# Performance work log

Hardware: AMD Instinct MI355X
Metric: run time of the kernel (lower is better)

Reference implementation:

```python
import jax, jax.numpy as jnp
import numpy as np
import math

# geometry: ROI [-140.8,-40,-3,140.8,40,1], grid 0.4 -> (Z,Y,X)=(10,200,704)
B_AG = 2              # total agents = 1 sample x 2 agents
Z, Y, X = 10, 200, 704
Z1, Y1, X1 = 5, 100, 352   # after stride-2 conv (k=3, p=1)
N_PTS = 10000         # active radar voxels per agent
C_IN, C0, C1 = 64, 32, 64
N_IN = B_AG * N_PTS
CAP0 = 27 * N_IN                # padded bound on spconv0 active outputs
CAP1 = B_AG * Z1 * Y1 * X1      # padded bound on spconv1 active outputs
EPS = 1e-5

_OFFS = np.array([[a, b, c] for a in range(3) for b in range(3) for c in range(3)])


def _spconv_rulebook(coords, stride, zyx, pair_cap, out_cap):
    """Rulebook for SparseConv3d k=3 pad=1. coords [N,4]=(b,z,y,x).
    Returns gather [27,P], scatter [27,P] (dummy=out_cap), out coords padded
    to out_cap (pad coords are out-of-bounds so dense scatter drops them)."""
    oz, oy, ox = zyx
    per_in, per_lin = [], []
    for off in _OFFS:
        t = coords[:, 1:] + 1 - off
        ok = (t % stride == 0).all(1)
        o = t // stride
        ok &= (o >= 0).all(1) & (o[:, 0] < oz) & (o[:, 1] < oy) & (o[:, 2] < ox)
        idx = np.nonzero(ok)[0]
        oc = o[idx]
        per_in.append(idx)
        per_lin.append(((coords[idx, 0] * oz + oc[:, 0]) * oy + oc[:, 1]) * ox + oc[:, 2])
    all_lin = np.unique(np.concatenate(per_lin))
    n_out = len(all_lin)
    g = np.zeros((27, pair_cap), np.int32)
    s = np.full((27, pair_cap), out_cap, np.int32)
    for k in range(27):
        n = len(per_in[k])
        g[k, :n] = per_in[k]
        s[k, :n] = np.searchsorted(all_lin, per_lin[k])
    b = all_lin // (oz * oy * ox); r = all_lin % (oz * oy * ox)
    zc = r // (oy * ox); r = r % (oy * ox)
    out_coords = np.stack([b, zc, r // ox, r % ox], 1).astype(np.int32)
    pad = np.zeros((out_cap - n_out, 4), np.int32); pad[:, 1] = oz  # OOB -> dropped
    return g, s, np.concatenate([out_coords, pad], 0), n_out


def _subm_rulebook(coords, n_act, zyx, pair_cap, out_cap):
    """SubMConv3d k=3: same active set in/out; coords[:n_act] sorted by lin id."""
    oz, oy, ox = zyx
    c = coords[:n_act]
    lins = ((c[:, 0] * oz + c[:, 1]) * oy + c[:, 2]) * ox + c[:, 3]
    g = np.zeros((27, pair_cap), np.int32)
    s = np.full((27, pair_cap), out_cap, np.int32)
    for k, off in enumerate(_OFFS):
        cand = c[:, 1:] + (off - 1)
        ok = (cand >= 0).all(1) & (cand[:, 0] < oz) & (cand[:, 1] < oy) & (cand[:, 2] < ox)
        cl = ((c[:, 0] * oz + cand[:, 0]) * oy + cand[:, 1]) * ox + cand[:, 2]
        pos = np.minimum(np.searchsorted(lins, cl), n_act - 1)
        ok &= lins[pos] == cl
        idx = np.nonzero(ok)[0]
        g[k, :len(idx)] = pos[idx]
        s[k, :len(idx)] = idx
    return g, s


def setup_inputs() -> dict:
    rng = np.random.default_rng(0)
    cl = []
    for b in range(B_AG):
        lin = np.sort(rng.choice(Z * Y * X, N_PTS, replace=False))
        z = lin // (Y * X); r = lin % (Y * X)
        cl.append(np.stack([np.full(N_PTS, b), z, r // X, r % X], 1))
    coords_in = np.concatenate(cl, 0).astype(np.int64)

    g0, s0, coords0, n0 = _spconv_rulebook(coords_in, 1, (Z, Y, X), N_IN, CAP0)
    ga, sa = _subm_rulebook(coords0, n0, (Z, Y, X), CAP0, CAP0)
    g1, s1, coords1, n1 = _spconv_rulebook(coords0[:n0], 2, (Z1, Y1, X1), CAP0, CAP1)
    gb, sb = _subm_rulebook(coords1, n1, (Z1, Y1, X1), CAP1, CAP1)

    ks = jax.random.split(jax.random.key(0), 20)
    f32 = jnp.float32
    def W(k, *shape, fan):
        return jax.random.normal(k, shape, f32) * (1.0 / np.sqrt(fan))
    def bn(k, c):  # [gamma, beta, running_mean, running_var]
        m = jax.random.normal(k, (c,), f32) * 0.1
        v = 1.0 + jax.random.uniform(jax.random.fold_in(k, 1), (c,), f32)
        return jnp.stack([jnp.ones((c,), f32), jnp.zeros((c,), f32), m, v])
    return dict(
        sp_feats=jax.random.normal(ks[0], (N_IN, C_IN), f32),
        w_in=W(ks[1], C_IN, C0, fan=C_IN),
        w0=W(ks[2], 27, C0, C0, fan=27 * C0), bnp0=bn(ks[3], C0),
        w0a=W(ks[4], 27, C0, C0, fan=27 * C0), bnp0a=bn(ks[5], C0),
        w0b=W(ks[6], 27, C0, C0, fan=27 * C0), bnp0b=bn(ks[7], C0),
        w1=W(ks[8], 27, C0, C1, fan=27 * C0), bnp1=bn(ks[9], C1),
        w1a=W(ks[10], 27, C1, C1, fan=27 * C1), bnp1a=bn(ks[11], C1),
        w1b=W(ks[12], 27, C1, C1, fan=27 * C1), bnp1b=bn(ks[13], C1),
        ct0_w=W(ks[14], C0 * Z, 64, 1, 1, fan=C0 * Z), ct0_b=jnp.zeros((64,), f32),
        bnt0=bn(ks[15], 64),
        ct1_w=W(ks[16], C1 * Z1, 64, 2, 2, fan=C1 * Z1 * 4), ct1_b=jnp.zeros((64,), f32),
        bnt1=bn(ks[17], 64),
        coords0=jnp.asarray(coords0), coords1=jnp.asarray(coords1),
        g0=jnp.asarray(g0), s0=jnp.asarray(s0),
        ga=jnp.asarray(ga), sa=jnp.asarray(sa),
        g1=jnp.asarray(g1), s1=jnp.asarray(s1),
        gb=jnp.asarray(gb), sb=jnp.asarray(sb),
        record_len=2,
    )


def _bn1d(x, p):  # x [N,C]; p [4,C]
    g, b, m, v = p
    return (x - m) * (g * jax.lax.rsqrt(v + EPS)) + b


def _bn2d(x, p):  # x [B,C,H,W]
    g, b, m, v = (t[:, None, None] for t in p)
    return (x - m) * (g * jax.lax.rsqrt(v + EPS)) + b


def _spconv(feats, g, s, W, out_cap):
    """gather-GEMM-scatter: feats [Nin,Cin], g/s [27,P], W [27,Cin,Cout]."""
    out = jnp.zeros((out_cap + 1, W.shape[2]), feats.dtype)  # +1 dummy row
    for k in range(27):
        out = out.at[s[k]].add(feats[g[k]] @ W[k])
    return out[:out_cap]


def _to_dense(feats, coords, b, z, y, x):
    d = jnp.zeros((b, z, y, x, feats.shape[1]), feats.dtype)
    d = d.at[coords[:, 0], coords[:, 1], coords[:, 2], coords[:, 3]].add(feats)
    return d.transpose(0, 4, 1, 2, 3)  # B,C,Z,Y,X


def _conv_t2d(x, w, b, stride, pad):
    """torch ConvTranspose2d; w [Cin,Cout,k,k]."""
    k = w.shape[2]
    wf = jnp.flip(w, (2, 3)).transpose(1, 0, 2, 3)  # Cout,Cin,k,k
    out = jax.lax.conv_general_dilated(
        x, wf, window_strides=(1, 1),
        padding=[(k - 1 - pad, k - 1 - pad)] * 2,
        lhs_dilation=(stride, stride),
        dimension_numbers=('NCHW', 'OIHW', 'NCHW'))
    return out + b[None, :, None, None]


def _att_fusion(x, L):
    """OpenCOOD AttFusion: per-pixel scaled dot-product attention over agents,
    keep ego (agent 0). Assumes uniform record_len == L."""
    B, C, H, Wd = x.shape
    S = B // L
    xr = x.reshape(S, L, C, H * Wd).transpose(0, 3, 1, 2)  # S,HW,L,C
    att = jax.nn.softmax(jnp.einsum('snlc,snmc->snlm', xr, xr) / math.sqrt(C), -1)
    h = jnp.einsum('snlm,snmc->snlc', att, xr)[:, :, 0, :]  # ego agent
    return h.transpose(0, 2, 1).reshape(S, C, H, Wd)


def reference(sp_feats, w_in, w0, bnp0, w0a, bnp0a, w0b, bnp0b,
              w1, bnp1, w1a, bnp1a, w1b, bnp1b,
              ct0_w, ct0_b, bnt0, ct1_w, ct1_b, bnt1,
              coords0, coords1, g0, s0, ga, sa, g1, s1, gb, sb, record_len):
    relu = jax.nn.relu
    f = sp_feats @ w_in                         # input_conv (k=1)
    # ---- encoder layer 0 (stride 1) ----
    f = relu(_bn1d(_spconv(f, g0, s0, w0, CAP0), bnp0))
    f = relu(_bn1d(_spconv(f, ga, sa, w0a, CAP0), bnp0a))
    f = relu(_bn1d(_spconv(f, ga, sa, w0b, CAP0), bnp0b))
    d0 = _to_dense(f, coords0, B_AG, Z, Y, X).reshape(B_AG, C0 * Z, Y, X)  # b (c z) y x
    bev0 = relu(_bn2d(_conv_t2d(d0, ct0_w, ct0_b, 1, 0), bnt0))
    bev0 = _att_fusion(bev0, record_len)
    # ---- encoder layer 1 (stride 2) ----
    f = relu(_bn1d(_spconv(f, g1, s1, w1, CAP1), bnp1))
    f = relu(_bn1d(_spconv(f, gb, sb, w1a, CAP1), bnp1a))
    f = relu(_bn1d(_spconv(f, gb, sb, w1b, CAP1), bnp1b))
    d1 = _to_dense(f, coords1, B_AG, Z1, Y1, X1).reshape(B_AG, C1 * Z1, Y1, X1)
    bev1 = relu(_bn2d(_conv_t2d(d1, ct1_w, ct1_b, 2, 0), bnt1))
    bev1 = _att_fusion(bev1, record_len)
    return jnp.concatenate([bev0, bev1], axis=1)  # [S, 128, 200, 704]
```

## Files before the change

### kernel.cpp

```cpp
#include <hip/hip_runtime.h>
#include <hip/hip_bf16.h>
#include <hip/hip_fp16.h>

#define N_PTS_IN   20000
#define CAP0C      540000
#define CAP1C      352000
#define ZD 10
#define YD 200
#define XD 704
#define Z1D 5
#define Y1D 100
#define X1D 352
#define HWOUT (YD*XD)

typedef _Float16 f16x8 __attribute__((ext_vector_type(8)));
typedef float    f32x4 __attribute__((ext_vector_type(4)));

__global__ __launch_bounds__(256) void gemm_in(const float* __restrict__ sp,
                                               const float* __restrict__ w,
                                               __half* __restrict__ fout) {
    int tid = blockIdx.x * 256 + threadIdx.x;
    int row = tid >> 3;
    int c4  = (tid & 7) * 4;
    if (row >= N_PTS_IN) return;
    float4 acc = {0.f, 0.f, 0.f, 0.f};
    const float* sr = sp + (size_t)row * 64;
#pragma unroll
    for (int ci = 0; ci < 64; ci += 4) {
        float4 fv = *(const float4*)(sr + ci);
        const float* wp = w + ci * 32 + c4;
        float4 w0 = *(const float4*)(wp);
        float4 w1 = *(const float4*)(wp + 32);
        float4 w2 = *(const float4*)(wp + 64);
        float4 w3 = *(const float4*)(wp + 96);
        acc.x += fv.x*w0.x + fv.y*w1.x + fv.z*w2.x + fv.w*w3.x;
        acc.y += fv.x*w0.y + fv.y*w1.y + fv.z*w2.y + fv.w*w3.y;
        acc.z += fv.x*w0.z + fv.y*w1.z + fv.z*w2.z + fv.w*w3.z;
        acc.w += fv.x*w0.w + fv.y*w1.w + fv.z*w2.w + fv.w*w3.w;
    }
    __half* fo = fout + (size_t)row * 32 + c4;
    fo[0] = __float2half(acc.x);
    fo[1] = __float2half(acc.y);
    fo[2] = __float2half(acc.z);
    fo[3] = __float2half(acc.w);
}

__global__ __launch_bounds__(256) void cvt_w(const float* __restrict__ src,
                                             __half* __restrict__ dst,
                                             int CIN, int COUT) {
    int i = blockIdx.x * 256 + threadIdx.x;
    if (i >= 27 * CIN * COUT) return;
    int ci = i % CIN;
    int t  = i / CIN;
    int co = t % COUT;
    int k  = t / COUT;
    dst[i] = __float2half(src[((size_t)k * CIN + ci) * COUT + co]);
}

__global__ __launch_bounds__(256) void cvt_ct0(const float* __restrict__ src,
                                               __half* __restrict__ dst) {
    int i = blockIdx.x * 256 + threadIdx.x;
    if (i >= 64 * 320) return;
    int zc = i % 320, co = i / 320;
    int z = zc >> 5, c = zc & 31;
    dst[i] = __float2half(src[(c * 10 + z) * 64 + co]);
}

__global__ __launch_bounds__(256) void cvt_ct1(const float* __restrict__ src,
                                               __half* __restrict__ dst) {
    int i = blockIdx.x * 256 + threadIdx.x;
    if (i >= 4 * 64 * 320) return;
    int zc = i % 320;
    int t  = i / 320;
    int co = t & 63;
    int kq = t >> 6;
    int z = zc >> 6, c = zc & 63;
    dst[i] = __float2half(src[((c * 5 + z) * 64 + co) * 4 + kq]);
}

__global__ __launch_bounds__(256) void build_nbr(const int* __restrict__ g,
                                                 const int* __restrict__ s,
                                                 int* __restrict__ nbrT,
                                                 int P, int cap) {
    int i = blockIdx.x * 256 + threadIdx.x;
    if (i >= 27 * P) return;
    int k = i / P, p = i - k * P;
    int sv = s[(size_t)k * P + p];
    if (sv >= cap) return;
    nbrT[(size_t)k * cap + sv] = g[(size_t)k * P + p];
}

__global__ __launch_bounds__(128) void find_nact(const int* __restrict__ c0,
                                                 const int* __restrict__ c1,
                                                 int* __restrict__ nA) {
    int t = threadIdx.x;
    if (t == 0) {
        int lo = 0, hi = CAP0C;
        while (lo < hi) {
            int mid = (lo + hi) >> 1;
            if (c0[4 * mid + 1] >= ZD) hi = mid; else lo = mid + 1;
        }
        nA[0] = lo;
    } else if (t == 64) {
        int lo = 0, hi = CAP1C;
        while (lo < hi) {
            int mid = (lo + hi) >> 1;
            if (c1[4 * mid + 1] >= Z1D) hi = mid; else lo = mid + 1;
        }
        nA[1] = lo;
    }
}

__global__ __launch_bounds__(256) void build_vox(const int* __restrict__ coords,
                                                 int* __restrict__ v2r,
                                                 int cap, int Zdim, int Ydim, int Xdim) {
    int r = blockIdx.x * 256 + threadIdx.x;
    if (r >= cap) return;
    int b = coords[4*r], z = coords[4*r+1], y = coords[4*r+2], x = coords[4*r+3];
    if (z >= Zdim) return;
    v2r[(((size_t)b * Zdim + z) * Ydim + y) * Xdim + x] = r;
}

template <int CIN, int COUT>
__global__ __launch_bounds__(256) void spconv_reg(const __half* __restrict__ f,
                                                  const __half* __restrict__ wt,
                                                  const float* __restrict__ bnp,
                                                  const int* __restrict__ nbrT,
                                                  __half* __restrict__ fout,
                                                  int ncap,
                                                  const int* __restrict__ nA) {
    constexpr int NT = COUT / 16;
    constexpr int KT = CIN / 32;
    constexpr int NCHUNK = CIN / 8;
    constexpr int MASK = NCHUNK - 1;
    constexpr int LCH  = (NCHUNK == 8) ? 3 : 2;
    constexpr int TILE_H = COUT * CIN;
    constexpr int TB = TILE_H * 2 / 256;
    constexpr int OST_H = 4 * 32 * COUT;
    constexpr int SH_H = (2 * TILE_H > OST_H) ? 2 * TILE_H : OST_H;
    __shared__ __align__(16) __half S[SH_H];

    int tid = threadIdx.x;
    int wv = tid >> 6, lane = tid & 63;
    int quad = lane >> 4, l16 = lane & 15;

    int bid = blockIdx.x;
    int nfull = (int)gridDim.x & ~63;
    int sb;
    if (bid < nfull) {
        int grp = bid >> 6, w = bid & 63;
        sb = grp * 64 + (w & 7) * 8 + (w >> 3);
    } else {
        sb = bid;
    }

    if (sb * 128 >= *nA) return;

    int m0 = sb * 128 + wv * 32;
    int r0 = m0 + l16;
    int r1 = m0 + 16 + l16;
    bool ok0 = r0 < ncap, ok1 = r1 < ncap;

    f32x4 acc[2][NT] = {};

    int gC0 = ok0 ? nbrT[r0] : -1;
    int gC1 = ok1 ? nbrT[r1] : -1;
    int gN0 = ok0 ? nbrT[(size_t)ncap + r0] : -1;
    int gN1 = ok1 ? nbrT[(size_t)ncap + r1] : -1;
    bool anyC = __ballot((gC0 >= 0) || (gC1 >= 0)) != 0ull;
    bool ever = false;

    f16x8 aC0[KT], aC1[KT];
#pragma unroll
    for (int kt = 0; kt < KT; ++kt) {
        uint4 z4 = {0u,0u,0u,0u};
        aC0[kt] = *(f16x8*)&z4;
        aC1[kt] = *(f16x8*)&z4;
    }
    if (anyC) {
        const __half* p0 = f + (size_t)((gC0 < 0) ? 0 : gC0) * CIN + quad * 8;
        const __half* p1 = f + (size_t)((gC1 < 0) ? 0 : gC1) * CIN + quad * 8;
#pragma unroll
        for (int kt = 0; kt < KT; ++kt) {
            uint4 u0 = {0u,0u,0u,0u}, u1 = {0u,0u,0u,0u};
            if (gC0 >= 0) u0 = *(const uint4*)(p0 + kt * 32);
            if (gC1 >= 0) u1 = *(const uint4*)(p1 + kt * 32);
            aC0[kt] = *(f16x8*)&u0;
            aC1[kt] = *(f16x8*)&u1;
        }
    }

    {
        const char* src = (const char*)(wt) + tid * TB;
        if constexpr (TB == 32) {
            uint4 w0 = *(const uint4*)src;
            uint4 w1 = *(const uint4*)(src + 16);
            int p0 = tid * 2;
#pragma unroll
            for (int j = 0; j < 2; ++j) {
                int p = p0 + j;
                int row = p >> LCH, c = p & MASK;
                *(uint4*)(S + (row * NCHUNK + (c ^ (row & MASK))) * 8) = (j ? w1 : w0);
            }
        } else if constexpr (TB == 16) {
            uint4 w0 = *(const uint4*)src;
            int p = tid;
            int row = p >> LCH, c = p & MASK;
            *(uint4*)(S + (row * NCHUNK + (c ^ (row & MASK))) * 8) = w0;
        } else {
            uint2 w0 = *(const uint2*)src;
            int p = tid >> 1, half = tid & 1;
            int row = p >> LCH, c = p & MASK;
            *(uint2*)(S + (row * NCHUNK + (c ^ (row & MASK))) * 8 + half * 4) = w0;
        }
    }
    __syncthreads();

#pragma unroll 1
    for (int k = 0; k < 27; ++k) {
        int gNN0 = -1, gNN1 = -1;
        if (k + 2 < 27) {
            if (ok0) gNN0 = nbrT[(size_t)(k + 2) * ncap + r0];
            if (ok1) gNN1 = nbrT[(size_t)(k + 2) * ncap + r1];
        }
        bool anyN = __ballot((gN0 >= 0) || (gN1 >= 0)) != 0ull;
        f16x8 aN0[KT], aN1[KT];
#pragma unroll
        for (int kt = 0; kt < KT; ++kt) {
            uint4 z4 = {0u,0u,0u,0u};
            aN0[kt] = *(f16x8*)&z4;
            aN1[kt] = *(f16x8*)&z4;
        }
        if (anyN) {
            const __half* p0 = f + (size_t)((gN0 < 0) ? 0 : gN0) * CIN + quad * 8;
            const __half* p1 = f + (size_t)((gN1 < 0) ? 0 : gN1) * CIN + quad * 8;
#pragma unroll
            for (int kt = 0; kt < KT; ++kt) {
                uint4 u0 = {0u,0u,0u,0u}, u1 = {0u,0u,0u,0u};
                if (gN0 >= 0) u0 = *(const uint4*)(p0 + kt * 32);
                if (gN1 >= 0) u1 = *(const uint4*)(p1 + kt * 32);
                aN0[kt] = *(f16x8*)&u0;
                aN1[kt] = *(f16x8*)&u1;
            }
        }
        bool doStage = (k + 1 < 27);
        uint4 w0{}, w1{}; uint2 w2{};
        if (doStage) {
            const char* src = (const char*)(wt + (size_t)(k + 1) * TILE_H) + tid * TB;
            if constexpr (TB == 32)      { w0 = *(const uint4*)src; w1 = *(const uint4*)(src + 16); }
            else if constexpr (TB == 16) { w0 = *(const uint4*)src; }
            else                         { w2 = *(const uint2*)src; }
        }
        if (anyC) {
            ever = true;
            const __half* Wb = S + (k & 1) * TILE_H;
#pragma unroll
            for (int kt = 0; kt < KT; ++kt) {
#pragma unroll
                for (int nt = 0; nt < NT; ++nt) {
                    int row = nt * 16 + l16;
                    int c   = kt * 4 + quad;
                    f16x8 b = *(const f16x8*)(Wb + (row * NCHUNK + (c ^ (row & MASK))) * 8);
                    acc[0][nt] = __builtin_amdgcn_mfma_f32_16x16x32_f16(aC0[kt], b, acc[0][nt], 0, 0, 0);
                    acc[1][nt] = __builtin_amdgcn_mfma_f32_16x16x32_f16(aC1[kt], b, acc[1][nt], 0, 0, 0);
                }
            }
        }
        if (doStage) {
            __half* dst = S + ((k + 1) & 1) * TILE_H;
            if constexpr (TB == 32) {
                int p0 = tid * 2;
#pragma unroll
                for (int j = 0; j < 2; ++j) {
                    int p = p0 + j;
                    int row = p >> LCH, c = p & MASK;
                    *(uint4*)(dst + (row * NCHUNK + (c ^ (row & MASK))) * 8) = (j ? w1 : w0);
                }
            } else if constexpr (TB == 16) {
                int p = tid;
                int row = p >> LCH, c = p & MASK;
                *(uint4*)(dst + (row * NCHUNK + (c ^ (row & MASK))) * 8) = w0;
            } else {
                int p = tid >> 1, half = tid & 1;
                int row = p >> LCH, c = p & MASK;
                *(uint2*)(dst + (row * NCHUNK + (c ^ (row & MASK))) * 8 + half * 4) = w2;
            }
        }
        asm volatile("s_waitcnt lgkmcnt(0)" ::: "memory");
        __builtin_amdgcn_s_barrier();
#pragma unroll
        for (int kt = 0; kt < KT; ++kt) { aC0[kt] = aN0[kt]; aC1[kt] = aN1[kt]; }
        anyC = anyN;
        gC0 = gN0; gC1 = gN1; gN0 = gNN0; gN1 = gNN1;
    }

    if (!ever) return;
    __half* O = S + wv * (32 * COUT);
#pragma unroll
    for (int nt = 0; nt < NT; ++nt) {
        int co = nt * 16 + l16;
        float g = bnp[co], b = bnp[COUT + co];
        float mn = bnp[2*COUT + co], vv = bnp[3*COUT + co];
        float s  = g * rsqrtf(vv + 1e-5f);
        float sh = b - mn * s;
#pragma unroll
        for (int m = 0; m < 2; ++m)
#pragma unroll
            for (int r_ = 0; r_ < 4; ++r_) {
                int row = m * 16 + quad * 4 + r_;
                O[row * COUT + co] = __float2half(fmaxf(acc[m][nt][r_] * s + sh, 0.f));
            }
    }
    constexpr int OCH = COUT / 8;
#pragma unroll
    for (int j = 0; j < 32 * OCH / 64; ++j) {
        int idx = j * 64 + lane;
        int r = idx / OCH, c = idx % OCH;
        if (m0 + r < ncap)
            *(uint4*)(fout + (size_t)(m0 + r) * COUT + c * 8) =
                *(const uint4*)(O + r * COUT + c * 8);
    }
}

__global__ __launch_bounds__(256) void bev0_mfma(const __half* __restrict__ f0,
                                                 const __half* __restrict__ wtT,
                                                 const float* __restrict__ bias,
                                                 const float* __restrict__ bnp,
                                                 const int* __restrict__ v2r,
                                                 float* __restrict__ out) {
    __shared__ float Ot[64][66];
    int tid = threadIdx.x;
    int y = blockIdx.x / 11, x0 = (blockIdx.x % 11) * 64;
    int wv = tid >> 6, lane = tid & 63;
    int quad = lane >> 4, l16 = lane & 15;

    int rz[2][10];
#pragma unroll
    for (int m = 0; m < 2; ++m) {
        int row = wv * 32 + m * 16 + l16;
        int b = row & 1, p = row >> 1;
#pragma unroll
        for (int z = 0; z < 10; ++z)
            rz[m][z] = v2r[((b * ZD + z) * YD + y) * XD + x0 + p];
    }

    f32x4 acc[2][4] = {};
    f16x8 aC[2], bC[4];
#pragma unroll
    for (int m = 0; m < 2; ++m) {
        uint4 u = {0u,0u,0u,0u};
        int r = rz[m][0];
        if (r >= 0) u = *(const uint4*)(f0 + (size_t)r * 32 + quad * 8);
        aC[m] = *(f16x8*)&u;
    }
#pragma unroll
    for (int nt = 0; nt < 4; ++nt)
        bC[nt] = *(const f16x8*)(wtT + (size_t)(nt * 16 + l16) * 320 + quad * 8);

#pragma unroll
    for (int ks = 0; ks < 10; ++ks) {
        f16x8 aN[2], bN[4];
        if (ks + 1 < 10) {
#pragma unroll
            for (int m = 0; m < 2; ++m) {
                uint4 u = {0u,0u,0u,0u};
                int r = rz[m][ks + 1];
                if (r >= 0) u = *(const uint4*)(f0 + (size_t)r * 32 + quad * 8);
                aN[m] = *(f16x8*)&u;
            }
#pragma unroll
            for (int nt = 0; nt < 4; ++nt)
                bN[nt] = *(const f16x8*)(wtT + (size_t)(nt * 16 + l16) * 320 + (ks + 1) * 32 + quad * 8);
        } else {
            uint4 z4 = {0u,0u,0u,0u};
#pragma unroll
            for (int m = 0; m < 2; ++m) aN[m] = *(f16x8*)&z4;
#pragma unroll
            for (int nt = 0; nt < 4; ++nt) bN[nt] = *(f16x8*)&z4;
        }
#pragma unroll
        for (int nt = 0; nt < 4; ++nt) {
            acc[0][nt] = __builtin_amdgcn_mfma_f32_16x16x32_f16(aC[0], bC[nt], acc[0][nt], 0, 0, 0);
            acc[1][nt] = __builtin_amdgcn_mfma_f32_16x16x32_f16(aC[1], bC[nt], acc[1][nt], 0, 0, 0);
        }
        aC[0] = aN[0]; aC[1] = aN[1];
#pragma unroll
        for (int nt = 0; nt < 4; ++nt) bC[nt] = bN[nt];
    }

#pragma unroll
    for (int nt = 0; nt < 4; ++nt) {
        int co = nt * 16 + l16;
        float s  = bnp[co] * rsqrtf(bnp[192 + co] + 1e-5f);
        float sh = (bias[co] - bnp[128 + co]) * s + bnp[64 + co];
#pragma unroll
        for (int m = 0; m < 2; ++m)
#pragma unroll
            for (int r_ = 0; r_ < 4; ++r_)
                acc[m][nt][r_] = fmaxf(acc[m][nt][r_] * s + sh, 0.f);
    }

#pragma unroll
    for (int m = 0; m < 2; ++m)
#pragma unroll
        for (int jj = 0; jj < 2; ++jj) {
            float s00 = 0.f, s01 = 0.f;
#pragma unroll
            for (int nt = 0; nt < 4; ++nt) {
                float xv0 = acc[m][nt][2 * jj], xv1 = acc[m][nt][2 * jj + 1];
                s00 += xv0 * xv0;
                s01 += xv0 * xv1;
            }
#pragma unroll
            for (int o = 8; o > 0; o >>= 1) {
                s00 += __shfl_xor(s00, o);
                s01 += __shfl_xor(s01, o);
            }
            float a0 = s00 * 0.125f, a1 = s01 * 0.125f;
            float mx = fmaxf(a0, a1);
            float e0 = expf(a0 - mx), e1 = expf(a1 - mx);
            float inv = 1.f / (e0 + e1);
            int pl = wv * 16 + m * 8 + quad * 2 + jj;
#pragma unroll
            for (int nt = 0; nt < 4; ++nt)
                Ot[nt * 16 + l16][pl] =
                    (e0 * acc[m][nt][2 * jj] + e1 * acc[m][nt][2 * jj + 1]) * inv;
        }
    __syncthreads();

#pragma unroll
    for (int i = 0; i < 16; ++i) {
        int idx = i * 256 + tid;
        int co = idx >> 6, px = idx & 63;
        out[(size_t)co * HWOUT + (size_t)y * XD + x0 + px] = Ot[co][px];
    }
}

__global__ __launch_bounds__(256) void bev1_mfma(const __half* __restrict__ f1,
                                                 const __half* __restrict__ wtT,
                                                 const float* __restrict__ bias,
                                                 const float* __restrict__ bnp,
                                                 const int* __restrict__ v2r,
                                                 float* __restrict__ out) {
    constexpr int WST = 328;
    __shared__ __align__(16) __half Wl[64 * WST];
    __shared__ float Ot[64][66];
    int tid = threadIdx.x;
    int bid = blockIdx.x;
    int ky = bid & 1;
    int t  = bid >> 1;
    int iy = t / 11, j0 = (t % 11) * 32;
    int wv = tid >> 6, lane = tid & 63;
    int quad = lane >> 4, l16 = lane & 15;

    int row = wv * 16 + l16;
    int b = row & 1, p = row >> 1;
    int rz[5];
#pragma unroll
    for (int z = 0; z < 5; ++z)
        rz[z] = v2r[((b * Z1D + z) * Y1D + iy) * X1D + j0 + p];

    f16x8 a[10];
#pragma unroll
    for (int ks = 0; ks < 10; ++ks) {
        int z = ks >> 1, hf = ks & 1;
        uint4 u = {0u,0u,0u,0u};
        int r = rz[z];
        if (r >= 0) u = *(const uint4*)(f1 + (size_t)r * 64 + hf * 32 + quad * 8);
        a[ks] = *(f16x8*)&u;
    }

    f32x4 acc[2][4] = {};
#pragma unroll 1
    for (int kx = 0; kx < 2; ++kx) {
        const __half* wk = wtT + (size_t)(ky * 2 + kx) * 64 * 320;
        if (kx) __syncthreads();
#pragma unroll
        for (int c = 0; c < 10; ++c) {
            int idx = c * 256 + tid;
            int r_ = idx / 40, col = idx % 40;
            uint4 v = *(const uint4*)(wk + r_ * 320 + col * 8);
            *(uint4*)(Wl + r_ * WST + col * 8) = v;
        }
        __syncthreads();
#pragma unroll
        for (int ks = 0; ks < 10; ++ks)
#pragma unroll
            for (int nt = 0; nt < 4; ++nt) {
                f16x8 bf = *(const f16x8*)(Wl + (nt * 16 + l16) * WST + ks * 32 + quad * 8);
                acc[kx][nt] = __builtin_amdgcn_mfma_f32_16x16x32_f16(a[ks], bf, acc[kx][nt], 0, 0, 0);
            }
    }

#pragma unroll
    for (int kx = 0; kx < 2; ++kx) {
#pragma unroll
        for (int nt = 0; nt < 4; ++nt) {
            int co = nt * 16 + l16;
            float s  = bnp[co] * rsqrtf(bnp[192 + co] + 1e-5f);
            float sh = (bias[co] - bnp[128 + co]) * s + bnp[64 + co];
#pragma unroll
            for (int r_ = 0; r_ < 4; ++r_)
                acc[kx][nt][r_] = fmaxf(acc[kx][nt][r_] * s + sh, 0.f);
        }
#pragma unroll
        for (int jj = 0; jj < 2; ++jj) {
            float s00 = 0.f, s01 = 0.f;
#pragma unroll
            for (int nt = 0; nt < 4; ++nt) {
                float xv0 = acc[kx][nt][2 * jj], xv1 = acc[kx][nt][2 * jj + 1];
                s00 += xv0 * xv0;
                s01 += xv0 * xv1;
            }
#pragma unroll
            for (int o = 8; o > 0; o >>= 1) {
                s00 += __shfl_xor(s00, o);
                s01 += __shfl_xor(s01, o);
            }
            float a0 = s00 * 0.125f, a1 = s01 * 0.125f;
            float mx = fmaxf(a0, a1);
            float e0 = expf(a0 - mx), e1 = expf(a1 - mx);
            float inv = 1.f / (e0 + e1);
            int pl = wv * 8 + quad * 2 + jj;
#pragma unroll
            for (int nt = 0; nt < 4; ++nt)
                Ot[nt * 16 + l16][2 * pl + kx] =
                    (e0 * acc[kx][nt][2 * jj] + e1 * acc[kx][nt][2 * jj + 1]) * inv;
        }
    }
    __syncthreads();

    int yo = 2 * iy + ky;
#pragma unroll
    for (int i = 0; i < 16; ++i) {
        int idx = i * 256 + tid;
        int co = idx >> 6, xx = idx & 63;
        out[(size_t)co * HWOUT + (size_t)yo * XD + 2 * j0 + xx] = Ot[co][xx];
    }
}

extern "C" void kernel_launch(void* const* d_in, const int* in_sizes, int n_in,
                              void* d_out, int out_size, void* d_ws, size_t ws_size,
                              hipStream_t stream) {
    const float* sp    = (const float*)d_in[0];
    const float* w_in  = (const float*)d_in[1];
    const float* w0    = (const float*)d_in[2];
    const float* bnp0  = (const float*)d_in[3];
    const float* w0a   = (const float*)d_in[4];
    const float* bnp0a = (const float*)d_in[5];
    const float* w0b   = (const float*)d_in[6];
    const float* bnp0b = (const float*)d_in[7];
    const float* w1    = (const float*)d_in[8];
    const float* bnp1  = (const float*)d_in[9];
    const float* w1a   = (const float*)d_in[10];
    const float* bnp1a = (const float*)d_in[11];
    const float* w1b   = (const float*)d_in[12];
    const float* bnp1b = (const float*)d_in[13];
    const float* ct0w  = (const float*)d_in[14];
    const float* ct0b  = (const float*)d_in[15];
    const float* bnt0  = (const float*)d_in[16];
    const float* ct1w  = (const float*)d_in[17];
    const float* ct1b  = (const float*)d_in[18];
    const float* bnt1  = (const float*)d_in[19];
    const int* coords0 = (const int*)d_in[20];
    const int* coords1 = (const int*)d_in[21];
    const int* g0 = (const int*)d_in[22];
    const int* s0 = (const int*)d_in[23];
    const int* ga = (const int*)d_in[24];
    const int* sa = (const int*)d_in[25];
    const int* g1 = (const int*)d_in[26];
    const int* s1 = (const int*)d_in[27];
    const int* gb = (const int*)d_in[28];
    const int* sb = (const int*)d_in[29];
    float* out = (float*)d_out;

    __half* fInH = (__half*)d_ws;
    __half* R1h  = fInH + 640000;
    __half* R2h  = R1h + 22528000;
    __half* wt0  = R2h + 22528000;
    __half* wt0a = wt0  + 27648;
    __half* wt0b = wt0a + 27648;
    __half* wt1  = wt0b + 27648;
    __half* wt1a = wt1  + 55296;
    __half* wt1b = wt1a + 110592;
    __half* wtT0 = wt1b + 110592;
    __half* wtT1 = wtT0 + 20480;
    int*   nbrT = (int*)(wtT1 + 81920);
    int*   v2r0 = nbrT;
    int*   v2r1 = nbrT + 2816000;
    int*   nAct = nbrT + 14580000;

    find_nact<<<1, 128, 0, stream>>>(coords0, coords1, nAct);
    cvt_w<<<(27*32*32 + 255) / 256, 256, 0, stream>>>(w0,  wt0,  32, 32);
    cvt_w<<<(27*32*32 + 255) / 256, 256, 0, stream>>>(w0a, wt0a, 32, 32);
    cvt_w<<<(27*32*32 + 255) / 256, 256, 0, stream>>>(w0b, wt0b, 32, 32);
    cvt_w<<<(27*32*64 + 255) / 256, 256, 0, stream>>>(w1,  wt1,  32, 64);
    cvt_w<<<(27*64*64 + 255) / 256, 256, 0, stream>>>(w1a, wt1a, 64, 64);
    cvt_w<<<(27*64*64 + 255) / 256, 256, 0, stream>>>(w1b, wt1b, 64, 64);
    cvt_ct0<<<(64*320 + 255) / 256, 256, 0, stream>>>(ct0w, wtT0);
    cvt_ct1<<<(4*64*320 + 255) / 256, 256, 0, stream>>>(ct1w, wtT1);

    gemm_in<<<(N_PTS_IN * 8 + 255) / 256, 256, 0, stream>>>(sp, w_in, fInH);

    hipMemsetAsync(nbrT, 0xFF, (size_t)CAP0C * 27 * 4, stream);
    build_nbr<<<(27 * N_PTS_IN + 255) / 256, 256, 0, stream>>>(g0, s0, nbrT, N_PTS_IN, CAP0C);
    spconv_reg<32, 32><<<(CAP0C + 127) / 128, 256, 0, stream>>>(fInH, wt0, bnp0, nbrT, R1h, CAP0C, nAct + 0);

    hipMemsetAsync(nbrT, 0xFF, (size_t)CAP0C * 27 * 4, stream);
    build_nbr<<<(27 * CAP0C + 255) / 256, 256, 0, stream>>>(ga, sa, nbrT, CAP0C, CAP0C);
    spconv_reg<32, 32><<<(CAP0C + 127) / 128, 256, 0, stream>>>(R1h, wt0a, bnp0a, nbrT, R2h, CAP0C, nAct + 0);
    spconv_reg<32, 32><<<(CAP0C + 127) / 128, 256, 0, stream>>>(R2h, wt0b, bnp0b, nbrT, R1h, CAP0C, nAct + 0);

    hipMemsetAsync(v2r0, 0xFF, (size_t)2816000 * 4, stream);
    build_vox<<<(CAP0C + 255) / 256, 256, 0, stream>>>(coords0, v2r0, CAP0C, ZD, YD, XD);
    bev0_mfma<<<YD * 11, 256, 0, stream>>>(R1h, wtT0, ct0b, bnt0, v2r0, out);

    hipMemsetAsync(nbrT, 0xFF, (size_t)CAP1C * 27 * 4, stream);
    build_nbr<<<(27 * CAP0C + 255) / 256, 256, 0, stream>>>(g1, s1, nbrT, CAP0C, CAP1C);
    spconv_reg<32, 64><<<(CAP1C + 127) / 128, 256, 0, stream>>>(R1h, wt1, bnp1, nbrT, R2h, CAP1C, nAct + 1);

    hipMemsetAsync(nbrT, 0xFF, (size_t)CAP1C * 27 * 4, stream);
    build_nbr<<<(27 * CAP1C + 255) / 256, 256, 0, stream>>>(gb, sb, nbrT, CAP1C, CAP1C);
    spconv_reg<64, 64><<<(CAP1C + 127) / 128, 256, 0, stream>>>(R2h, wt1a, bnp1a, nbrT, R1h, CAP1C, nAct + 1);
    spconv_reg<64, 64><<<(CAP1C + 127) / 128, 256, 0, stream>>>(R1h, wt1b, bnp1b, nbrT, R2h, CAP1C, nAct + 1);

    hipMemsetAsync(v2r1, 0xFF, (size_t)352000 * 4, stream);
    build_vox<<<(CAP1C + 255) / 256, 256, 0, stream>>>(coords1, v2r1, CAP1C, Z1D, Y1D, X1D);
    bev1_mfma<<<Y1D * 11 * 2, 256, 0, stream>>>(R2h, wtT1, ct1b, bnt1, v2r1, out + (size_t)64 * HWOUT);
}
```

Before: 915.2 us.

## Add 32x32 sparse conv kernel holding all 27 weight taps in shared memory

Adds a specialized spconv kernel for the 32->32 layers. It loads all 27 fp16 weight tiles into XOR-swizzled LDS once per block, then loops over the kernel offsets with neighbor indices and gathered features prefetched one to two steps ahead. Wave-level ballots skip MFMA work for offsets with no neighbors, and blocks are remapped so they are visited in a different order. The cost is 54KB of LDS per block, which limits occupancy, in exchange for removing per-offset weight reloads and synchronisation.

```diff
diff --git a/kernel.cpp b/kernel.cpp
--- a/kernel.cpp
+++ b/kernel.cpp
@@ -119,6 +119,130 @@
     int b = coords[4*r], z = coords[4*r+1], y = coords[4*r+2], x = coords[4*r+3];
     if (z >= Zdim) return;
     v2r[(((size_t)b * Zdim + z) * Ydim + y) * Xdim + x] = r;
+}
+
+__global__ __launch_bounds__(256) void spconv_allw(const __half* __restrict__ f,
+                                                   const __half* __restrict__ wt,
+                                                   const float* __restrict__ bnp,
+                                                   const int* __restrict__ nbrT,
+                                                   __half* __restrict__ fout,
+                                                   int ncap,
+                                                   const int* __restrict__ nA) {
+    __shared__ __align__(16) __half W[27 * 1024];
+
+    int tid = threadIdx.x;
+    int wv = tid >> 6, lane = tid & 63;
+    int quad = lane >> 4, l16 = lane & 15;
+
+    int bid = blockIdx.x;
+    int nfull = (int)gridDim.x & ~63;
+    int sb;
+    if (bid < nfull) {
+        int grp = bid >> 6, w = bid & 63;
+        sb = grp * 64 + (w & 7) * 8 + (w >> 3);
+    } else {
+        sb = bid;
+    }
+
+    if (sb * 128 >= *nA) return;
+
+    int m0 = sb * 128 + wv * 32;
+    int r0 = m0 + l16;
+    int r1 = m0 + 16 + l16;
+    bool ok0 = r0 < ncap, ok1 = r1 < ncap;
+
+    f32x4 acc[2][2] = {};
+
+    int gC0 = ok0 ? nbrT[r0] : -1;
+    int gC1 = ok1 ? nbrT[r1] : -1;
+    int gN0 = ok0 ? nbrT[(size_t)ncap + r0] : -1;
+    int gN1 = ok1 ? nbrT[(size_t)ncap + r1] : -1;
+    bool anyC = __ballot((gC0 >= 0) || (gC1 >= 0)) != 0ull;
+    bool ever = false;
+
+#pragma unroll
+    for (int j = 0; j < 14; ++j) {
+        int idx = j * 256 + tid;
+        if (idx < 3456) {
+            uint4 v = *(const uint4*)((const char*)wt + (size_t)idx * 16);
+            int k  = idx >> 7, p = idx & 127;
+            int row = p >> 2, c = p & 3;
+            *(uint4*)(W + k * 1024 + (row * 4 + (c ^ (row & 3))) * 8) = v;
+        }
+    }
+
+    f16x8 aC0, aC1;
+    {
+        uint4 u0 = {0u,0u,0u,0u}, u1 = {0u,0u,0u,0u};
+        if (anyC) {
+            if (gC0 >= 0) u0 = *(const uint4*)(f + (size_t)gC0 * 32 + quad * 8);
+            if (gC1 >= 0) u1 = *(const uint4*)(f + (size_t)gC1 * 32 + quad * 8);
+        }
+        aC0 = *(f16x8*)&u0;
+        aC1 = *(f16x8*)&u1;
+    }
+    __syncthreads();
+
+#pragma unroll 1
+    for (int k = 0; k < 27; ++k) {
+        int gNN0 = -1, gNN1 = -1;
+        if (k + 2 < 27) {
+            if (ok0) gNN0 = nbrT[(size_t)(k + 2) * ncap + r0];
+            if (ok1) gNN1 = nbrT[(size_t)(k + 2) * ncap + r1];
+        }
+        bool anyN = __ballot((gN0 >= 0) || (gN1 >= 0)) != 0ull;
+        f16x8 aN0, aN1;
+        {
+            uint4 u0 = {0u,0u,0u,0u}, u1 = {0u,0u,0u,0u};
+            if (anyN) {
+                if (gN0 >= 0) u0 = *(const uint4*)(f + (size_t)gN0 * 32 + quad * 8);
+                if (gN1 >= 0) u1 = *(const uint4*)(f + (size_t)gN1 * 32 + quad * 8);
+            }
+            aN0 = *(f16x8*)&u0;
+            aN1 = *(f16x8*)&u1;
+        }
+        if (anyC) {
+            ever = true;
+            const __half* Wb = W + k * 1024;
+#pragma unroll
+            for (int nt = 0; nt < 2; ++nt) {
+                int row = nt * 16 + l16;
+                f16x8 b = *(const f16x8*)(Wb + (row * 4 + (quad ^ (row & 3))) * 8);
+                acc[0][nt] = __builtin_amdgcn_mfma_f32_16x16x32_f16(aC0, b, acc[0][nt], 0, 0, 0);
+                acc[1][nt] = __builtin_amdgcn_mfma_f32_16x16x32_f16(aC1, b, acc[1][nt], 0, 0, 0);
+            }
+        }
+        aC0 = aN0; aC1 = aN1;
+        anyC = anyN;
+        gC0 = gN0; gC1 = gN1; gN0 = gNN0; gN1 = gNN1;
+    }
+
+    __syncthreads();
+    if (!ever) return;
+    __half* O = W + wv * 1024;
+#pragma unroll
+    for (int nt = 0; nt < 2; ++nt) {
+        int co = nt * 16 + l16;
+        float g = bnp[co], b = bnp[32 + co];
+        float mn = bnp[64 + co], vv = bnp[96 + co];
+        float s  = g * rsqrtf(vv + 1e-5f);
+        float sh = b - mn * s;
+#pragma unroll
+        for (int m = 0; m < 2; ++m)
+#pragma unroll
+            for (int r_ = 0; r_ < 4; ++r_) {
+                int row = m * 16 + quad * 4 + r_;
+                O[row * 32 + co] = __float2half(fmaxf(acc[m][nt][r_] * s + sh, 0.f));
+            }
+    }
+#pragma unroll
+    for (int j = 0; j < 2; ++j) {
+        int idx = j * 64 + lane;
+        int r = idx >> 2, c = idx & 3;
+        if (m0 + r < ncap)
+            *(uint4*)(fout + (size_t)(m0 + r) * 32 + c * 8) =
+                *(const uint4*)(O + r * 32 + c * 8);
+    }
 }
 
 template <int CIN, int COUT>
@@ -604,12 +728,12 @@
 
     hipMemsetAsync(nbrT, 0xFF, (size_t)CAP0C * 27 * 4, stream);
     build_nbr<<<(27 * N_PTS_IN + 255) / 256, 256, 0, stream>>>(g0, s0, nbrT, N_PTS_IN, CAP0C);
-    spconv_reg<32, 32><<<(CAP0C + 127) / 128, 256, 0, stream>>>(fInH, wt0, bnp0, nbrT, R1h, CAP0C, nAct + 0);
+    spconv_allw<<<(CAP0C + 127) / 128, 256, 0, stream>>>(fInH, wt0, bnp0, nbrT, R1h, CAP0C, nAct + 0);
 
     hipMemsetAsync(nbrT, 0xFF, (size_t)CAP0C * 27 * 4, stream);
     build_nbr<<<(27 * CAP0C + 255) / 256, 256, 0, stream>>>(ga, sa, nbrT, CAP0C, CAP0C);
-    spconv_reg<32, 32><<<(CAP0C + 127) / 128, 256, 0, stream>>>(R1h, wt0a, bnp0a, nbrT, R2h, CAP0C, nAct + 0);
-    spconv_reg<32, 32><<<(CAP0C + 127) / 128, 256, 0, stream>>>(R2h, wt0b, bnp0b, nbrT, R1h, CAP0C, nAct + 0);
+    spconv_allw<<<(CAP0C + 127) / 128, 256, 0, stream>>>(R1h, wt0a, bnp0a, nbrT, R2h, CAP0C, nAct + 0);
+    spconv_allw<<<(CAP0C + 127) / 128, 256, 0, stream>>>(R2h, wt0b, bnp0b, nbrT, R1h, CAP0C, nAct + 0);
 
     hipMemsetAsync(v2r0, 0xFF, (size_t)2816000 * 4, stream);
     build_vox<<<(CAP0C + 255) / 256, 256, 0, stream>>>(coords0, v2r0, CAP0C, ZD, YD, XD);
```

Result: slower. 1.075 ms (+17.4%).
